# Kernel tuning notes

Measured on AMD Instinct MI355X. Metric: run time of the kernel, lower is better.

Reference implementation:

```python
import jax, jax.numpy as jnp
import numpy as np

N = 100000  # nodes
E = 1600000  # directed edges

_DIMS = [("eg1", 3, 160), ("eg2", 160, 80), ("eg3", 80, 40), ("eg4", 40, 20),
         ("el1", 20, 10), ("el2", 10, 3), ("dl1", 3, 10), ("dl2", 10, 20),
         ("dg1", 20, 40), ("dg2", 40, 80), ("dg3", 80, 160), ("dg4", 160, 3)]


def _lin_init(key, ci, co):
    s = 1.0 / np.sqrt(ci)
    kw, kb = jax.random.split(key)
    w = jax.random.uniform(kw, (ci, co), jnp.float32, -s, s)
    b = jax.random.uniform(kb, (co,), jnp.float32, -s, s)
    return w, b


def setup_inputs():
    key = jax.random.key(0)
    k0, k1, k2 = jax.random.split(key, 3)
    x = jax.random.normal(k0, (N, 3), jnp.float32)
    src = jax.random.randint(k1, (E,), 0, N)
    dst = jax.random.randint(k2, (E,), 0, N)
    edge_index = jnp.stack([src, dst])  # [2, E] int32 indices
    out = {"x": x, "edge_index": edge_index}
    for i, (name, ci, co) in enumerate(_DIMS):
        w, b = _lin_init(jax.random.fold_in(key, i + 10), ci, co)
        out[name + "_w"] = w
        out[name + "_b"] = b
    return out


def _gcn(x, w, b, src, dst, norm):
    # PyG GCNConv: linear transform, then symmetric-normalized scatter-add.
    h = x @ w
    agg = jax.ops.segment_sum(h[src] * norm[:, None], dst, num_segments=N)
    return agg + b


def reference(x, edge_index, eg1_w, eg1_b, eg2_w, eg2_b, eg3_w, eg3_b, eg4_w, eg4_b,
              el1_w, el1_b, el2_w, el2_b, dl1_w, dl1_b, dl2_w, dl2_b,
              dg1_w, dg1_b, dg2_w, dg2_b, dg3_w, dg3_b, dg4_w, dg4_b):
    loops = jnp.arange(N)
    src = jnp.concatenate([edge_index[0], loops])  # add self-loops (PyG default)
    dst = jnp.concatenate([edge_index[1], loops])
    deg = jax.ops.segment_sum(jnp.ones(src.shape[0], x.dtype), dst, num_segments=N)
    dis = jnp.where(deg > 0, jax.lax.rsqrt(deg), 0.0)
    norm = dis[src] * dis[dst]  # D^-1/2 A D^-1/2 edge weights
    relu = jax.nn.relu
    h = relu(_gcn(x, eg1_w, eg1_b, src, dst, norm))
    h = relu(_gcn(h, eg2_w, eg2_b, src, dst, norm))
    h = relu(_gcn(h, eg3_w, eg3_b, src, dst, norm))
    h = relu(_gcn(h, eg4_w, eg4_b, src, dst, norm))
    h = relu(h @ el1_w + el1_b)
    h = h @ el2_w + el2_b  # latent [N, 3]
    h = relu(h @ dl1_w + dl1_b)
    h = relu(h @ dl2_w + dl2_b)
    h = relu(_gcn(h, dg1_w, dg1_b, src, dst, norm))
    h = relu(_gcn(h, dg2_w, dg2_b, src, dst, norm))
    h = relu(_gcn(h, dg3_w, dg3_b, src, dst, norm))
    h = jnp.tanh(_gcn(h, dg4_w, dg4_b, src, dst, norm))
    return h
```

## Files before the change

### kernel.cpp

```cpp
#include <hip/hip_runtime.h>
#include <hip/hip_fp16.h>
#include <math.h>

#define BS 256
static constexpr int NN = 100000;
static constexpr int EE = 1600000;
static constexpr int BUCKET_SH = 7;
static constexpr int NBUCKET = (NN + 127) >> BUCKET_SH;
static constexpr int NB_PART = 256;
static constexpr int CHUNK = EE / NB_PART;
static constexpr int NP = NBUCKET * NB_PART;
static constexpr int SCAN_ELEMS = 1024;
static constexpr int NPB = (NP + SCAN_ELEMS - 1) / SCAN_ELEMS;

static inline int cdiv(long long a, int b) { return (int)((a + b - 1) / b); }

template <int ACT>
__device__ __forceinline__ float act_f(float v) {
    if (ACT == 1) return fmaxf(v, 0.0f);
    if (ACT == 2) return tanhf(v);
    return v;
}

__device__ __forceinline__ unsigned short h16(float v) {
    return __half_as_ushort(__float2half(v));
}
__device__ __forceinline__ unsigned pack2h(float a, float b) {
    return (unsigned)h16(a) | ((unsigned)h16(b) << 16);
}
__device__ __forceinline__ float4 cvt4h(uint2 r) {
    float2 fa = __half22float2(*(const __half2*)&r.x);
    float2 fb = __half22float2(*(const __half2*)&r.y);
    return make_float4(fa.x, fa.y, fb.x, fb.y);
}
__device__ __forceinline__ void acc8h(uint4 r, float4& a, float4& b) {
    float2 f0 = __half22float2(*(const __half2*)&r.x);
    float2 f1 = __half22float2(*(const __half2*)&r.y);
    float2 f2 = __half22float2(*(const __half2*)&r.z);
    float2 f3 = __half22float2(*(const __half2*)&r.w);
    a.x += f0.x; a.y += f0.y; a.z += f1.x; a.w += f1.y;
    b.x += f2.x; b.y += f2.y; b.z += f3.x; b.w += f3.y;
}

template <int OUTM>
__device__ __forceinline__ void store1(float* out, size_t idx, float v, float dn) {
    if (OUTM == 0) out[idx] = v;
    else if (OUTM == 1) out[idx] = v * dn;
    else if (OUTM == 2) ((unsigned short*)out)[idx] = h16(v * dn);
    else ((unsigned short*)out)[idx] = h16(v);
}

__global__ __launch_bounds__(256) void k_hist(const int* __restrict__ dst,
                                              int* __restrict__ part_cnt) {
    __shared__ int h[NBUCKET];
    int b = blockIdx.x;
    for (int j = threadIdx.x; j < NBUCKET; j += 256) h[j] = 0;
    __syncthreads();
    int e0 = b * CHUNK;
    for (int k = threadIdx.x; k < CHUNK; k += 256)
        atomicAdd(&h[dst[e0 + k] >> BUCKET_SH], 1);
    __syncthreads();
    for (int j = threadIdx.x; j < NBUCKET; j += 256)
        part_cnt[j * NB_PART + b] = h[j];
}

__global__ void k_scanA(const int* __restrict__ in, int* __restrict__ outp,
                        int* __restrict__ bsums) {
    __shared__ int lds[BS];
    int base = blockIdx.x * SCAN_ELEMS;
    int t = threadIdx.x;
    int v[4];
    int s = 0;
#pragma unroll
    for (int j = 0; j < 4; ++j) {
        int idx = base + t * 4 + j;
        v[j] = (idx < NP) ? in[idx] : 0;
        s += v[j];
    }
    lds[t] = s;
    __syncthreads();
    for (int off = 1; off < BS; off <<= 1) {
        int add = (t >= off) ? lds[t - off] : 0;
        __syncthreads();
        lds[t] += add;
        __syncthreads();
    }
    int run = lds[t] - s;
    if (t == BS - 1) bsums[blockIdx.x] = lds[BS - 1];
#pragma unroll
    for (int j = 0; j < 4; ++j) {
        int idx = base + t * 4 + j;
        if (idx < NP) outp[idx] = run;
        run += v[j];
    }
}

__global__ void k_scanB(int* __restrict__ bsums) {
    if (threadIdx.x == 0 && blockIdx.x == 0) {
        int acc = 0;
        for (int i = 0; i < NPB; ++i) {
            int t = bsums[i];
            bsums[i] = acc;
            acc += t;
        }
    }
}

__global__ void k_scanC(int* __restrict__ outp, const int* __restrict__ bsums,
                        int* __restrict__ bbase) {
    int i = blockIdx.x * BS + threadIdx.x;
    if (i < NP) {
        int v = outp[i] + bsums[i / SCAN_ELEMS];
        outp[i] = v;
        if ((i & (NB_PART - 1)) == 0) bbase[i / NB_PART] = v;
    }
    if (i == 0) bbase[NBUCKET] = EE;
}

__global__ __launch_bounds__(256) void k_part(const int* __restrict__ src,
                                              const int* __restrict__ dst,
                                              const int* __restrict__ scan_out,
                                              unsigned* __restrict__ epb) {
    __shared__ int cur[NBUCKET];
    int b = blockIdx.x;
    for (int j = threadIdx.x; j < NBUCKET; j += 256) cur[j] = scan_out[j * NB_PART + b];
    __syncthreads();
    int e0 = b * CHUNK;
    for (int k = threadIdx.x; k < CHUNK; k += 256) {
        int e = e0 + k;
        int d = dst[e];
        int s = src[e];
        int pos = atomicAdd(&cur[d >> BUCKET_SH], 1);
        epb[pos] = ((unsigned)(d & ((1 << BUCKET_SH) - 1)) << 17) | (unsigned)s;
    }
}

__global__ __launch_bounds__(256) void k_fine2(const int* __restrict__ bbase,
                                               const unsigned* __restrict__ epb,
                                               int* __restrict__ eidx,
                                               int* __restrict__ rowptr,
                                               float* __restrict__ dis) {
    __shared__ int hcnt[1 << BUCKET_SH];
    __shared__ int hoff[1 << BUCKET_SH];
    int b = blockIdx.x;
    int n0 = b << BUCKET_SH;
    int nloc = min(1 << BUCKET_SH, NN - n0);
    int t = threadIdx.x;
    if (t < (1 << BUCKET_SH)) hcnt[t] = 0;
    __syncthreads();
    int es = bbase[b], ee = bbase[b + 1];
    for (int k = es + t; k < ee; k += 256) atomicAdd(&hcnt[epb[k] >> 17], 1);
    __syncthreads();
    if (t < (1 << BUCKET_SH)) hoff[t] = hcnt[t];
    __syncthreads();
    for (int off = 1; off < (1 << BUCKET_SH); off <<= 1) {
        int add = (t >= off && t < (1 << BUCKET_SH)) ? hoff[t - off] : 0;
        __syncthreads();
        if (t < (1 << BUCKET_SH)) hoff[t] += add;
        __syncthreads();
    }
    if (t < nloc) {
        int excl = hoff[t] - hcnt[t];
        rowptr[n0 + t] = es + excl;
        dis[n0 + t] = rsqrtf((float)(hcnt[t] + 1));
    }
    __syncthreads();
    if (t < (1 << BUCKET_SH)) hoff[t] = es + hoff[t] - hcnt[t];
    __syncthreads();
    for (int k = es + t; k < ee; k += 256) {
        unsigned p = epb[k];
        int pos = atomicAdd(&hoff[p >> 17], 1);
        eidx[pos] = (int)(p & 0x1FFFFu);
    }
    if (b == NBUCKET - 1 && t == 0) rowptr[NN] = EE;
}

template <int C, int ACT, bool HASB>
__global__ void k_gatherw(const unsigned short* __restrict__ g, const int* __restrict__ rowptr,
                          const int* __restrict__ eidx, const float* __restrict__ dis,
                          const float* __restrict__ b, float* __restrict__ out) {
    static_assert(C % 8 == 0, "C%8");
    constexpr int V = C / 8;
    int t = blockIdx.x * BS + threadIdx.x;
    if (t >= NN * V) return;
    int n = t / V, v = t % V;
    const uint4* g4 = (const uint4*)g;
    float4 accA = make_float4(0.f, 0.f, 0.f, 0.f);
    float4 accB = make_float4(0.f, 0.f, 0.f, 0.f);
    acc8h(g4[(size_t)n * V + v], accA, accB);
    int rs = rowptr[n], re = rowptr[n + 1];
    int k = rs;
    for (; k + 4 <= re; k += 4) {
        int s0 = eidx[k + 0], s1 = eidx[k + 1], s2 = eidx[k + 2], s3 = eidx[k + 3];
        uint4 r0 = g4[(size_t)s0 * V + v];
        uint4 r1 = g4[(size_t)s1 * V + v];
        uint4 r2 = g4[(size_t)s2 * V + v];
        uint4 r3 = g4[(size_t)s3 * V + v];
        acc8h(r0, accA, accB);
        acc8h(r1, accA, accB);
        acc8h(r2, accA, accB);
        acc8h(r3, accA, accB);
    }
    for (; k < re; ++k) {
        acc8h(g4[(size_t)eidx[k] * V + v], accA, accB);
    }
    float dn = dis[n];
    accA.x *= dn; accA.y *= dn; accA.z *= dn; accA.w *= dn;
    accB.x *= dn; accB.y *= dn; accB.z *= dn; accB.w *= dn;
    if (HASB) {
        float4 b0 = ((const float4*)b)[v * 2 + 0];
        float4 b1 = ((const float4*)b)[v * 2 + 1];
        accA.x += b0.x; accA.y += b0.y; accA.z += b0.z; accA.w += b0.w;
        accB.x += b1.x; accB.y += b1.y; accB.z += b1.z; accB.w += b1.w;
    }
    accA.x = act_f<ACT>(accA.x); accA.y = act_f<ACT>(accA.y);
    accA.z = act_f<ACT>(accA.z); accA.w = act_f<ACT>(accA.w);
    accB.x = act_f<ACT>(accB.x); accB.y = act_f<ACT>(accB.y);
    accB.z = act_f<ACT>(accB.z); accB.w = act_f<ACT>(accB.w);
    float4* op = (float4*)out + (size_t)n * (C / 4) + v * 2;
    op[0] = accA;
    op[1] = accB;
}

template <int C, int ACT, bool HASB>
__global__ void k_gatherh(const unsigned short* __restrict__ g, const int* __restrict__ rowptr,
                          const int* __restrict__ eidx, const float* __restrict__ dis,
                          const float* __restrict__ b, float* __restrict__ out) {
    static_assert(C % 4 == 0, "C%4");
    constexpr int V = C / 4;
    int t = blockIdx.x * BS + threadIdx.x;
    if (t >= NN * V) return;
    int n = t / V, v = t % V;
    const uint2* g2 = (const uint2*)g;
    float4 acc = cvt4h(g2[(size_t)n * V + v]);
    int rs = rowptr[n], re = rowptr[n + 1];
    int k = rs;
    for (; k + 4 <= re; k += 4) {
        int s0 = eidx[k + 0], s1 = eidx[k + 1], s2 = eidx[k + 2], s3 = eidx[k + 3];
        uint2 r0 = g2[(size_t)s0 * V + v];
        uint2 r1 = g2[(size_t)s1 * V + v];
        uint2 r2 = g2[(size_t)s2 * V + v];
        uint2 r3 = g2[(size_t)s3 * V + v];
        float4 h0 = cvt4h(r0), h1 = cvt4h(r1), h2 = cvt4h(r2), h3 = cvt4h(r3);
        acc.x += (h0.x + h1.x) + (h2.x + h3.x);
        acc.y += (h0.y + h1.y) + (h2.y + h3.y);
        acc.z += (h0.z + h1.z) + (h2.z + h3.z);
        acc.w += (h0.w + h1.w) + (h2.w + h3.w);
    }
    for (; k < re; ++k) {
        float4 hv = cvt4h(g2[(size_t)eidx[k] * V + v]);
        acc.x += hv.x; acc.y += hv.y; acc.z += hv.z; acc.w += hv.w;
    }
    float dn = dis[n];
    acc.x *= dn; acc.y *= dn; acc.z *= dn; acc.w *= dn;
    if (HASB) {
        float4 bb = ((const float4*)b)[v];
        acc.x += bb.x; acc.y += bb.y; acc.z += bb.z; acc.w += bb.w;
    }
    acc.x = act_f<ACT>(acc.x);
    acc.y = act_f<ACT>(acc.y);
    acc.z = act_f<ACT>(acc.z);
    acc.w = act_f<ACT>(acc.w);
    ((float4*)out)[(size_t)n * V + v] = acc;
}

template <int ACT, bool HASB>
__global__ void k_gather3d(const float* __restrict__ g, const int* __restrict__ rowptr,
                           const int* __restrict__ eidx, const float* __restrict__ dis,
                           const float* __restrict__ b, float* __restrict__ out) {
    int n = blockIdx.x * BS + threadIdx.x;
    if (n >= NN) return;
    const float* gp = g + (size_t)n * 3;
    float a0 = gp[0], a1 = gp[1], a2 = gp[2];
    int rs = rowptr[n], re = rowptr[n + 1];
    int k = rs;
    for (; k + 4 <= re; k += 4) {
        const float* q0 = g + (size_t)eidx[k + 0] * 3;
        const float* q1 = g + (size_t)eidx[k + 1] * 3;
        const float* q2 = g + (size_t)eidx[k + 2] * 3;
        const float* q3 = g + (size_t)eidx[k + 3] * 3;
        float b00 = q0[0], b01 = q0[1], b02 = q0[2];
        float b10 = q1[0], b11 = q1[1], b12 = q1[2];
        float b20 = q2[0], b21 = q2[1], b22 = q2[2];
        float b30 = q3[0], b31 = q3[1], b32 = q3[2];
        a0 += (b00 + b10) + (b20 + b30);
        a1 += (b01 + b11) + (b21 + b31);
        a2 += (b02 + b12) + (b22 + b32);
    }
    for (; k < re; ++k) {
        const float* gq = g + (size_t)eidx[k] * 3;
        a0 += gq[0]; a1 += gq[1]; a2 += gq[2];
    }
    float dn = dis[n];
    a0 *= dn; a1 *= dn; a2 *= dn;
    if (HASB) { a0 += b[0]; a1 += b[1]; a2 += b[2]; }
    float* op = out + (size_t)n * 3;
    op[0] = act_f<ACT>(a0);
    op[1] = act_f<ACT>(a1);
    op[2] = act_f<ACT>(a2);
}

__global__ void k_scale3(const float* __restrict__ x, const float* __restrict__ dis,
                         float* __restrict__ g) {
    int i = blockIdx.x * BS + threadIdx.x;
    if (i < NN * 3) g[i] = x[i] * dis[i / 3];
}

template <int CIN, int COUT, int TC, int TN, int TM, int BK, int ACT, bool HASB, int OUTM, bool INH>
__global__ __launch_bounds__(256) void k_mm_tiled(const float* __restrict__ x,
                                                  const float* __restrict__ w,
                                                  const float* __restrict__ b,
                                                  float* __restrict__ out,
                                                  const float* __restrict__ dis) {
    constexpr int TR = 256 / TC;
    constexpr int BM = TR * TM;
    constexpr int LDA = BM + 4;
    constexpr int CHUNKS = CIN / BK;
    constexpr int BK4 = BK / 4;
    constexpr int CIN4 = CIN / 4;
    static_assert(TC * TN == COUT, "cols");
    static_assert(CIN % BK == 0 && BK % 4 == 0, "bk");
    static_assert(TM == 4 || TM == 8, "tm");
    __shared__ float As[BK * LDA];
    __shared__ float Ws[BK * COUT];
    const int tid = threadIdx.x;
    const int tc = tid % TC, tr = tid / TC;
    const int n0 = blockIdx.x * BM;

    float acc[TM][TN];
#pragma unroll
    for (int r = 0; r < TM; ++r)
#pragma unroll
        for (int j = 0; j < TN; ++j) acc[r][j] = HASB ? b[tc * TN + j] : 0.0f;

    const float4* x4 = (const float4*)x;
    const uint2* xh = (const uint2*)x;
    const float4* w4 = (const float4*)w;

    for (int ch = 0; ch < CHUNKS; ++ch) {
        const int kb4 = ch * BK4;
        if (ch) __syncthreads();
        for (int i = tid; i < BM * BK4; i += 256) {
            int r = i / BK4, k4 = i % BK4;
            int row = n0 + r;
            float4 v = make_float4(0.f, 0.f, 0.f, 0.f);
            if (row < NN) {
                if (INH) v = cvt4h(xh[(size_t)row * CIN4 + kb4 + k4]);
                else v = x4[(size_t)row * CIN4 + kb4 + k4];
            }
            int base = (4 * k4) * LDA + r;
            As[base] = v.x;
            As[base + LDA] = v.y;
            As[base + 2 * LDA] = v.z;
            As[base + 3 * LDA] = v.w;
        }
        for (int i = tid; i < BK * COUT / 4; i += 256) {
            ((float4*)Ws)[i] = w4[(size_t)kb4 * COUT + i];
        }
        __syncthreads();
#pragma unroll 4
        for (int k = 0; k < BK; ++k) {
            float a[TM];
            *(float4*)&a[0] = *(const float4*)&As[k * LDA + tr * TM];
            if (TM == 8) *(float4*)&a[4] = *(const float4*)&As[k * LDA + tr * TM + 4];
            float wr[TN];
#pragma unroll
            for (int j = 0; j < TN; ++j) wr[j] = Ws[k * COUT + tc * TN + j];
#pragma unroll
            for (int r = 0; r < TM; ++r)
#pragma unroll
                for (int j = 0; j < TN; ++j) acc[r][j] = fmaf(a[r], wr[j], acc[r][j]);
        }
    }
#pragma unroll
    for (int r = 0; r < TM; ++r) {
        int row = n0 + tr * TM + r;
        if (row < NN) {
            float dn = (OUTM == 1 || OUTM == 2) ? dis[row] : 0.0f;
            size_t base = (size_t)row * COUT + tc * TN;
#pragma unroll
            for (int j = 0; j < TN; ++j) store1<OUTM>(out, base + j, act_f<ACT>(acc[r][j]), dn);
        }
    }
}

template <int CIN, int COUT, int ACT, bool HASB, int OUTM>
__global__ void k_mm_vec4(const float* __restrict__ x, const float* __restrict__ w,
                          const float* __restrict__ b, float* __restrict__ out,
                          const float* __restrict__ dis) {
    static_assert(CIN % 4 == 0 && COUT % 4 == 0, "align");
    constexpr int TM = 8;
    constexpr int CIN4 = CIN / 4;
    constexpr int COUT4 = COUT / 4;
    constexpr int RG = NN / TM;
    int i = blockIdx.x * BS + threadIdx.x;
    if (i >= RG * COUT4) return;
    int c4 = i % COUT4;
    int n0 = (i / COUT4) * TM;
    const float4* x4 = (const float4*)x;
    const float4* w4 = (const float4*)w;
    float4 acc[TM];
    float4 bb = HASB ? ((const float4*)b)[c4] : make_float4(0.f, 0.f, 0.f, 0.f);
#pragma unroll
    for (int r = 0; r < TM; ++r) acc[r] = bb;
    for (int k4 = 0; k4 < CIN4; ++k4) {
        float4 wv[4];
#pragma unroll
        for (int j = 0; j < 4; ++j) wv[j] = w4[(size_t)(4 * k4 + j) * COUT4 + c4];
#pragma unroll
        for (int r = 0; r < TM; ++r) {
            float4 xv = x4[(size_t)(n0 + r) * CIN4 + k4];
            acc[r].x = fmaf(xv.x, wv[0].x, fmaf(xv.y, wv[1].x, fmaf(xv.z, wv[2].x, fmaf(xv.w, wv[3].x, acc[r].x))));
            acc[r].y = fmaf(xv.x, wv[0].y, fmaf(xv.y, wv[1].y, fmaf(xv.z, wv[2].y, fmaf(xv.w, wv[3].y, acc[r].y))));
            acc[r].z = fmaf(xv.x, wv[0].z, fmaf(xv.y, wv[1].z, fmaf(xv.z, wv[2].z, fmaf(xv.w, wv[3].z, acc[r].z))));
            acc[r].w = fmaf(xv.x, wv[0].w, fmaf(xv.y, wv[1].w, fmaf(xv.z, wv[2].w, fmaf(xv.w, wv[3].w, acc[r].w))));
        }
    }
#pragma unroll
    for (int r = 0; r < TM; ++r) {
        float vx = act_f<ACT>(acc[r].x), vy = act_f<ACT>(acc[r].y);
        float vz = act_f<ACT>(acc[r].z), vw = act_f<ACT>(acc[r].w);
        size_t gi = (size_t)(n0 + r) * COUT4 + c4;
        if (OUTM == 2) {
            float dn = dis[n0 + r];
            uint2 u;
            u.x = pack2h(vx * dn, vy * dn);
            u.y = pack2h(vz * dn, vw * dn);
            ((uint2*)out)[gi] = u;
        } else if (OUTM == 1) {
            float dn = dis[n0 + r];
            ((float4*)out)[gi] = make_float4(vx * dn, vy * dn, vz * dn, vw * dn);
        } else {
            ((float4*)out)[gi] = make_float4(vx, vy, vz, vw);
        }
    }
}

template <int CIN, int COUT, int ACT, int OUTM>
__global__ void k_mm_rowbcast(const float* __restrict__ x, const float* __restrict__ w,
                              const float* __restrict__ b, float* __restrict__ out) {
    static_assert(COUT % 4 == 0, "c4");
    constexpr int COUT4 = COUT / 4;
    int i = blockIdx.x * BS + threadIdx.x;
    if (i >= NN * COUT4) return;
    int n = i / COUT4, c4 = i % COUT4;
    const float4* w4 = (const float4*)w;
    float4 acc = ((const float4*)b)[c4];
    const float* xr = x + (size_t)n * CIN;
#pragma unroll
    for (int ci = 0; ci < CIN; ++ci) {
        float xv = xr[ci];
        float4 wv = w4[ci * COUT4 + c4];
        acc.x = fmaf(xv, wv.x, acc.x);
        acc.y = fmaf(xv, wv.y, acc.y);
        acc.z = fmaf(xv, wv.z, acc.z);
        acc.w = fmaf(xv, wv.w, acc.w);
    }
    acc.x = act_f<ACT>(acc.x); acc.y = act_f<ACT>(acc.y);
    acc.z = act_f<ACT>(acc.z); acc.w = act_f<ACT>(acc.w);
    if (OUTM == 3) {
        uint2 u;
        u.x = pack2h(acc.x, acc.y);
        u.y = pack2h(acc.z, acc.w);
        ((uint2*)out)[(size_t)n * COUT4 + c4] = u;
    } else {
        ((float4*)out)[(size_t)n * COUT4 + c4] = acc;
    }
}

template <int CIN, int COUT, int ACT, bool HASB, int OUTM>
__global__ void k_mm_simple(const float* __restrict__ x, const float* __restrict__ w,
                            const float* __restrict__ b, float* __restrict__ out,
                            const float* __restrict__ dis) {
    int i = blockIdx.x * BS + threadIdx.x;
    if (i >= NN * COUT) return;
    int n = i / COUT, c = i % COUT;
    const float* xr = x + (size_t)n * CIN;
    float acc = HASB ? b[c] : 0.0f;
#pragma unroll
    for (int ci = 0; ci < CIN; ++ci) acc = fmaf(xr[ci], w[ci * COUT + c], acc);
    float dn = (OUTM == 1 || OUTM == 2) ? dis[n] : 0.0f;
    store1<OUTM>(out, (size_t)i, act_f<ACT>(acc), dn);
}

template <int CIN, int COUT, int ACT, bool HASB, int OUTM, bool INH>
__global__ void k_mm_vec(const float* __restrict__ x, const float* __restrict__ w,
                         const float* __restrict__ b, float* __restrict__ out,
                         const float* __restrict__ dis) {
    static_assert(CIN % 4 == 0, "CIN%4");
    constexpr int TM = 8;
    constexpr int CIN4 = CIN / 4;
    constexpr int RG = NN / TM;
    int i = blockIdx.x * BS + threadIdx.x;
    if (i >= RG * COUT) return;
    int c = i % COUT;
    int n0 = (i / COUT) * TM;
    float acc[TM];
    float bb = HASB ? b[c] : 0.0f;
#pragma unroll
    for (int r = 0; r < TM; ++r) acc[r] = bb;
    const float4* x4 = (const float4*)x;
    const uint2* xh = (const uint2*)x;
    for (int k = 0; k < CIN4; ++k) {
        float w0 = w[(4 * k + 0) * COUT + c];
        float w1 = w[(4 * k + 1) * COUT + c];
        float w2 = w[(4 * k + 2) * COUT + c];
        float w3 = w[(4 * k + 3) * COUT + c];
#pragma unroll
        for (int r = 0; r < TM; ++r) {
            float4 xv;
            if (INH) xv = cvt4h(xh[(size_t)(n0 + r) * CIN4 + k]);
            else xv = x4[(size_t)(n0 + r) * CIN4 + k];
            acc[r] = fmaf(xv.x, w0, fmaf(xv.y, w1, fmaf(xv.z, w2, fmaf(xv.w, w3, acc[r]))));
        }
    }
#pragma unroll
    for (int r = 0; r < TM; ++r) {
        int row = n0 + r;
        float dn = (OUTM == 1 || OUTM == 2) ? dis[row] : 0.0f;
        store1<OUTM>(out, (size_t)row * COUT + c, act_f<ACT>(acc[r]), dn);
    }
}

extern "C" void kernel_launch(void* const* d_in, const int* in_sizes, int n_in,
                              void* d_out, int out_size, void* d_ws, size_t ws_size,
                              hipStream_t stream) {
    const float* x = (const float*)d_in[0];
    const int* ei = (const int*)d_in[1];
    const int* src = ei;
    const int* dst = ei + EE;
    const float* eg1_w = (const float*)d_in[2];  const float* eg1_b = (const float*)d_in[3];
    const float* eg2_w = (const float*)d_in[4];  const float* eg2_b = (const float*)d_in[5];
    const float* eg3_w = (const float*)d_in[6];  const float* eg3_b = (const float*)d_in[7];
    const float* eg4_w = (const float*)d_in[8];  const float* eg4_b = (const float*)d_in[9];
    const float* el1_w = (const float*)d_in[10]; const float* el1_b = (const float*)d_in[11];
    const float* el2_w = (const float*)d_in[12]; const float* el2_b = (const float*)d_in[13];
    const float* dl1_w = (const float*)d_in[14]; const float* dl1_b = (const float*)d_in[15];
    const float* dl2_w = (const float*)d_in[16]; const float* dl2_b = (const float*)d_in[17];
    const float* dg1_w = (const float*)d_in[18]; const float* dg1_b = (const float*)d_in[19];
    const float* dg2_w = (const float*)d_in[20]; const float* dg2_b = (const float*)d_in[21];
    const float* dg3_w = (const float*)d_in[22]; const float* dg3_b = (const float*)d_in[23];
    const float* dg4_w = (const float*)d_in[24]; const float* dg4_b = (const float*)d_in[25];
    float* out = (float*)d_out;

    char* ws = (char*)d_ws;
    size_t off = 0;
    auto alloc = [&](size_t bytes) {
        void* p = ws + off;
        off += (bytes + 15) & ~(size_t)15;
        return p;
    };
    int* part_cnt = (int*)alloc(sizeof(int) * NP);
    int* scan_out = (int*)alloc(sizeof(int) * NP);
    int* bsums    = (int*)alloc(sizeof(int) * NPB);
    int* bbase    = (int*)alloc(sizeof(int) * (NBUCKET + 1));
    int* rowptr   = (int*)alloc(sizeof(int) * (NN + 1));
    float* dis    = (float*)alloc(sizeof(float) * NN);
    int* eidx     = (int*)alloc(sizeof(int) * EE);
    unsigned* epb = (unsigned*)alloc(sizeof(unsigned) * EE);
    unsigned short* G = (unsigned short*)alloc(sizeof(unsigned short) * 80 * (size_t)NN);
    float* bufA = (float*)alloc(sizeof(float) * 160 * (size_t)NN);
    float* bufB = (float*)alloc(sizeof(float) * 160 * (size_t)NN);

    k_hist<<<NB_PART, 256, 0, stream>>>(dst, part_cnt);
    k_scanA<<<NPB, BS, 0, stream>>>(part_cnt, scan_out, bsums);
    k_scanB<<<1, 64, 0, stream>>>(bsums);
    k_scanC<<<cdiv(NP, BS), BS, 0, stream>>>(scan_out, bsums, bbase);
    k_part<<<NB_PART, 256, 0, stream>>>(src, dst, scan_out, epb);
    k_fine2<<<NBUCKET, 256, 0, stream>>>(bbase, epb, eidx, rowptr, dis);

    k_scale3<<<cdiv(3LL * NN, BS), BS, 0, stream>>>(x, dis, bufB);
    k_gather3d<0, false><<<cdiv(NN, BS), BS, 0, stream>>>(bufB, rowptr, eidx, dis, nullptr, bufA);
    k_mm_rowbcast<3, 160, 1, 3><<<cdiv(NN * 40LL, BS), BS, 0, stream>>>(bufA, eg1_w, eg1_b, bufB);

    k_mm_tiled<160, 80, 16, 5, 8, 32, 0, false, 2, true><<<cdiv(NN, 128), 256, 0, stream>>>(
        bufB, eg2_w, nullptr, (float*)G, dis);
    k_gatherw<80, 1, true><<<cdiv(NN * 10LL, BS), BS, 0, stream>>>(G, rowptr, eidx, dis, eg2_b, bufA);

    k_mm_tiled<80, 40, 8, 5, 4, 40, 0, false, 2, false><<<cdiv(NN, 128), 256, 0, stream>>>(
        bufA, eg3_w, nullptr, (float*)G, dis);
    k_gatherw<40, 1, true><<<cdiv(NN * 5LL, BS), BS, 0, stream>>>(G, rowptr, eidx, dis, eg3_b, bufB);

    k_mm_vec4<40, 20, 0, false, 2><<<cdiv((NN / 8) * 5LL, BS), BS, 0, stream>>>(
        bufB, eg4_w, nullptr, (float*)G, dis);
    k_gatherh<20, 1, true><<<cdiv(NN * 5LL, BS), BS, 0, stream>>>(G, rowptr, eidx, dis, eg4_b, bufA);

    k_mm_vec<20, 10, 1, true, 0, false><<<cdiv((NN / 8) * 10LL, BS), BS, 0, stream>>>(bufA, el1_w, el1_b, bufB, nullptr);
    k_mm_simple<10, 3, 0, true, 0><<<cdiv(3LL * NN, BS), BS, 0, stream>>>(bufB, el2_w, el2_b, bufA, nullptr);
    k_mm_simple<3, 10, 1, true, 0><<<cdiv(10LL * NN, BS), BS, 0, stream>>>(bufA, dl1_w, dl1_b, bufB, nullptr);
    k_mm_simple<10, 20, 1, true, 2><<<cdiv(20LL * NN, BS), BS, 0, stream>>>(bufB, dl2_w, dl2_b, (float*)G, dis);

    k_gatherh<20, 0, false><<<cdiv(NN * 5LL, BS), BS, 0, stream>>>(G, rowptr, eidx, dis, nullptr, bufA);
    k_mm_vec4<20, 40, 1, true, 2><<<cdiv((NN / 8) * 10LL, BS), BS, 0, stream>>>(
        bufA, dg1_w, dg1_b, (float*)G, dis);

    k_gatherw<40, 0, false><<<cdiv(NN * 5LL, BS), BS, 0, stream>>>(G, rowptr, eidx, dis, nullptr, bufB);
    k_mm_tiled<40, 80, 16, 5, 8, 40, 1, true, 2, false><<<cdiv(NN, 128), 256, 0, stream>>>(
        bufB, dg2_w, dg2_b, (float*)G, dis);

    k_gatherw<80, 0, false><<<cdiv(NN * 10LL, BS), BS, 0, stream>>>(G, rowptr, eidx, dis, nullptr, bufA);
    k_mm_tiled<80, 160, 32, 5, 8, 40, 1, true, 3, false><<<cdiv(NN, 64), 256, 0, stream>>>(
        bufA, dg3_w, dg3_b, bufB, nullptr);

    k_mm_vec<160, 3, 0, false, 1, true><<<cdiv((NN / 8) * 3LL, BS), BS, 0, stream>>>(bufB, dg4_w, nullptr, bufA, dis);
    k_gather3d<2, true><<<cdiv(NN, BS), BS, 0, stream>>>(bufA, rowptr, eidx, dis, dg4_b, out);
}
```

Measured before the change: 630.2 us.

## Store gather outputs as fp16 and fuse the latent MLP chain into one kernel

Gather kernels gain an option to write their aggregated activations as packed half precision, and the following matmul kernels read fp16 input. This roughly halves intermediate activation traffic between the gather and linear stages. The four small dense layers in the latent bottleneck are merged into one kernel that keeps weights in shared memory and intermediates in registers, which removes three launches and their round trips through global memory. The cost is more fp16 rounding of the activations, which may affect accuracy.

```diff
diff --git a/kernel.cpp b/kernel.cpp
--- a/kernel.cpp
+++ b/kernel.cpp
@@ -175,7 +175,7 @@
     if (b == NBUCKET - 1 && t == 0) rowptr[NN] = EE;
 }
 
-template <int C, int ACT, bool HASB>
+template <int C, int ACT, bool HASB, bool OUTH>
 __global__ void k_gatherw(const unsigned short* __restrict__ g, const int* __restrict__ rowptr,
                           const int* __restrict__ eidx, const float* __restrict__ dis,
                           const float* __restrict__ b, float* __restrict__ out) {
@@ -217,12 +217,21 @@
     accA.z = act_f<ACT>(accA.z); accA.w = act_f<ACT>(accA.w);
     accB.x = act_f<ACT>(accB.x); accB.y = act_f<ACT>(accB.y);
     accB.z = act_f<ACT>(accB.z); accB.w = act_f<ACT>(accB.w);
-    float4* op = (float4*)out + (size_t)n * (C / 4) + v * 2;
-    op[0] = accA;
-    op[1] = accB;
-}
-
-template <int C, int ACT, bool HASB>
+    if (OUTH) {
+        uint4 u;
+        u.x = pack2h(accA.x, accA.y);
+        u.y = pack2h(accA.z, accA.w);
+        u.z = pack2h(accB.x, accB.y);
+        u.w = pack2h(accB.z, accB.w);
+        ((uint4*)out)[(size_t)n * V + v] = u;
+    } else {
+        float4* op = (float4*)out + (size_t)n * (C / 4) + v * 2;
+        op[0] = accA;
+        op[1] = accB;
+    }
+}
+
+template <int C, int ACT, bool HASB, bool OUTH>
 __global__ void k_gatherh(const unsigned short* __restrict__ g, const int* __restrict__ rowptr,
                           const int* __restrict__ eidx, const float* __restrict__ dis,
                           const float* __restrict__ b, float* __restrict__ out) {
@@ -261,7 +270,14 @@
     acc.y = act_f<ACT>(acc.y);
     acc.z = act_f<ACT>(acc.z);
     acc.w = act_f<ACT>(acc.w);
-    ((float4*)out)[(size_t)n * V + v] = acc;
+    if (OUTH) {
+        uint2 u;
+        u.x = pack2h(acc.x, acc.y);
+        u.y = pack2h(acc.z, acc.w);
+        ((uint2*)out)[(size_t)n * V + v] = u;
+    } else {
+        ((float4*)out)[(size_t)n * V + v] = acc;
+    }
 }
 
 template <int ACT, bool HASB>
@@ -306,6 +322,78 @@
     if (i < NN * 3) g[i] = x[i] * dis[i / 3];
 }
 
+__global__ __launch_bounds__(256) void k_latent(const unsigned short* __restrict__ in20,
+                                                const float* __restrict__ el1_w, const float* __restrict__ el1_b,
+                                                const float* __restrict__ el2_w, const float* __restrict__ el2_b,
+                                                const float* __restrict__ dl1_w, const float* __restrict__ dl1_b,
+                                                const float* __restrict__ dl2_w, const float* __restrict__ dl2_b,
+                                                const float* __restrict__ dis,
+                                                unsigned short* __restrict__ G) {
+    __shared__ float w1[200], b1[10], w2[30], b2[3], w3[30], b3[10], w4[200], b4[20];
+    int t = threadIdx.x;
+    if (t < 200) w1[t] = el1_w[t];
+    if (t < 10) b1[t] = el1_b[t];
+    if (t < 30) w2[t] = el2_w[t];
+    if (t < 3) b2[t] = el2_b[t];
+    if (t < 30) w3[t] = dl1_w[t];
+    if (t < 10) b3[t] = dl1_b[t];
+    if (t < 200) w4[t] = dl2_w[t];
+    if (t < 20) b4[t] = dl2_b[t];
+    __syncthreads();
+    int n = blockIdx.x * 256 + t;
+    if (n >= NN) return;
+    float h0[20];
+    const uint2* ip = (const uint2*)in20 + (size_t)n * 5;
+#pragma unroll
+    for (int v = 0; v < 5; ++v) {
+        float4 f = cvt4h(ip[v]);
+        h0[v * 4 + 0] = f.x; h0[v * 4 + 1] = f.y;
+        h0[v * 4 + 2] = f.z; h0[v * 4 + 3] = f.w;
+    }
+    float a1[10];
+#pragma unroll
+    for (int j = 0; j < 10; ++j) {
+        float s = b1[j];
+#pragma unroll
+        for (int i = 0; i < 20; ++i) s = fmaf(h0[i], w1[i * 10 + j], s);
+        a1[j] = fmaxf(s, 0.0f);
+    }
+    float a2[3];
+#pragma unroll
+    for (int j = 0; j < 3; ++j) {
+        float s = b2[j];
+#pragma unroll
+        for (int i = 0; i < 10; ++i) s = fmaf(a1[i], w2[i * 3 + j], s);
+        a2[j] = s;
+    }
+    float a3[10];
+#pragma unroll
+    for (int j = 0; j < 10; ++j) {
+        float s = b3[j];
+#pragma unroll
+        for (int i = 0; i < 3; ++i) s = fmaf(a2[i], w3[i * 10 + j], s);
+        a3[j] = fmaxf(s, 0.0f);
+    }
+    float dn = dis[n];
+    uint2* gp = (uint2*)G + (size_t)n * 5;
+#pragma unroll
+    for (int v = 0; v < 5; ++v) {
+        float o[4];
+#pragma unroll
+        for (int q = 0; q < 4; ++q) {
+            int j = v * 4 + q;
+            float s = b4[j];
+#pragma unroll
+            for (int i = 0; i < 10; ++i) s = fmaf(a3[i], w4[i * 20 + j], s);
+            o[q] = fmaxf(s, 0.0f) * dn;
+        }
+        uint2 u;
+        u.x = pack2h(o[0], o[1]);
+        u.y = pack2h(o[2], o[3]);
+        gp[v] = u;
+    }
+}
+
 template <int CIN, int COUT, int TC, int TN, int TM, int BK, int ACT, bool HASB, int OUTM, bool INH>
 __global__ __launch_bounds__(256) void k_mm_tiled(const float* __restrict__ x,
                                                   const float* __restrict__ w,
@@ -384,7 +472,7 @@
     }
 }
 
-template <int CIN, int COUT, int ACT, bool HASB, int OUTM>
+template <int CIN, int COUT, int ACT, bool HASB, int OUTM, bool INH>
 __global__ void k_mm_vec4(const float* __restrict__ x, const float* __restrict__ w,
                           const float* __restrict__ b, float* __restrict__ out,
                           const float* __restrict__ dis) {
@@ -398,6 +486,7 @@
     int c4 = i % COUT4;
     int n0 = (i / COUT4) * TM;
     const float4* x4 = (const float4*)x;
+    const uint2* xh = (const uint2*)x;
     const float4* w4 = (const float4*)w;
     float4 acc[TM];
     float4 bb = HASB ? ((const float4*)b)[c4] : make_float4(0.f, 0.f, 0.f, 0.f);
@@ -409,7 +498,9 @@
         for (int j = 0; j < 4; ++j) wv[j] = w4[(size_t)(4 * k4 + j) * COUT4 + c4];
 #pragma unroll
         for (int r = 0; r < TM; ++r) {
-            float4 xv = x4[(size_t)(n0 + r) * CIN4 + k4];
+            float4 xv;
+            if (INH) xv = cvt4h(xh[(size_t)(n0 + r) * CIN4 + k4]);
+            else xv = x4[(size_t)(n0 + r) * CIN4 + k4];
             acc[r].x = fmaf(xv.x, wv[0].x, fmaf(xv.y, wv[1].x, fmaf(xv.z, wv[2].x, fmaf(xv.w, wv[3].x, acc[r].x))));
             acc[r].y = fmaf(xv.x, wv[0].y, fmaf(xv.y, wv[1].y, fmaf(xv.z, wv[2].y, fmaf(xv.w, wv[3].y, acc[r].y))));
             acc[r].z = fmaf(xv.x, wv[0].z, fmaf(xv.y, wv[1].z, fmaf(xv.z, wv[2].z, fmaf(xv.w, wv[3].z, acc[r].z))));
@@ -466,21 +557,6 @@
     } else {
         ((float4*)out)[(size_t)n * COUT4 + c4] = acc;
     }
-}
-
-template <int CIN, int COUT, int ACT, bool HASB, int OUTM>
-__global__ void k_mm_simple(const float* __restrict__ x, const float* __restrict__ w,
-                            const float* __restrict__ b, float* __restrict__ out,
-                            const float* __restrict__ dis) {
-    int i = blockIdx.x * BS + threadIdx.x;
-    if (i >= NN * COUT) return;
-    int n = i / COUT, c = i % COUT;
-    const float* xr = x + (size_t)n * CIN;
-    float acc = HASB ? b[c] : 0.0f;
-#pragma unroll
-    for (int ci = 0; ci < CIN; ++ci) acc = fmaf(xr[ci], w[ci * COUT + c], acc);
-    float dn = (OUTM == 1 || OUTM == 2) ? dis[n] : 0.0f;
-    store1<OUTM>(out, (size_t)i, act_f<ACT>(acc), dn);
 }
 
 template <int CIN, int COUT, int ACT, bool HASB, int OUTM, bool INH>
@@ -575,31 +651,29 @@
 
     k_mm_tiled<160, 80, 16, 5, 8, 32, 0, false, 2, true><<<cdiv(NN, 128), 256, 0, stream>>>(
         bufB, eg2_w, nullptr, (float*)G, dis);
-    k_gatherw<80, 1, true><<<cdiv(NN * 10LL, BS), BS, 0, stream>>>(G, rowptr, eidx, dis, eg2_b, bufA);
-
-    k_mm_tiled<80, 40, 8, 5, 4, 40, 0, false, 2, false><<<cdiv(NN, 128), 256, 0, stream>>>(
+    k_gatherw<80, 1, true, true><<<cdiv(NN * 10LL, BS), BS, 0, stream>>>(G, rowptr, eidx, dis, eg2_b, bufA);
+
+    k_mm_tiled<80, 40, 8, 5, 4, 40, 0, false, 2, true><<<cdiv(NN, 128), 256, 0, stream>>>(
         bufA, eg3_w, nullptr, (float*)G, dis);
-    k_gatherw<40, 1, true><<<cdiv(NN * 5LL, BS), BS, 0, stream>>>(G, rowptr, eidx, dis, eg3_b, bufB);
-
-    k_mm_vec4<40, 20, 0, false, 2><<<cdiv((NN / 8) * 5LL, BS), BS, 0, stream>>>(
+    k_gatherw<40, 1, true, true><<<cdiv(NN * 5LL, BS), BS, 0, stream>>>(G, rowptr, eidx, dis, eg3_b, bufB);
+
+    k_mm_vec4<40, 20, 0, false, 2, true><<<cdiv((NN / 8) * 5LL, BS), BS, 0, stream>>>(
         bufB, eg4_w, nullptr, (float*)G, dis);
-    k_gatherh<20, 1, true><<<cdiv(NN * 5LL, BS), BS, 0, stream>>>(G, rowptr, eidx, dis, eg4_b, bufA);
-
-    k_mm_vec<20, 10, 1, true, 0, false><<<cdiv((NN / 8) * 10LL, BS), BS, 0, stream>>>(bufA, el1_w, el1_b, bufB, nullptr);
-    k_mm_simple<10, 3, 0, true, 0><<<cdiv(3LL * NN, BS), BS, 0, stream>>>(bufB, el2_w, el2_b, bufA, nullptr);
-    k_mm_simple<3, 10, 1, true, 0><<<cdiv(10LL * NN, BS), BS, 0, stream>>>(bufA, dl1_w, dl1_b, bufB, nullptr);
-    k_mm_simple<10, 20, 1, true, 2><<<cdiv(20LL * NN, BS), BS, 0, stream>>>(bufB, dl2_w, dl2_b, (float*)G, dis);
-
-    k_gatherh<20, 0, false><<<cdiv(NN * 5LL, BS), BS, 0, stream>>>(G, rowptr, eidx, dis, nullptr, bufA);
-    k_mm_vec4<20, 40, 1, true, 2><<<cdiv((NN / 8) * 10LL, BS), BS, 0, stream>>>(
+    k_gatherh<20, 1, true, true><<<cdiv(NN * 5LL, BS), BS, 0, stream>>>(G, rowptr, eidx, dis, eg4_b, bufA);
+
+    k_latent<<<cdiv(NN, 256), 256, 0, stream>>>((const unsigned short*)bufA,
+        el1_w, el1_b, el2_w, el2_b, dl1_w, dl1_b, dl2_w, dl2_b, dis, G);
+
+    k_gatherh<20, 0, false, true><<<cdiv(NN * 5LL, BS), BS, 0, stream>>>(G, rowptr, eidx, dis, nullptr, bufA);
+    k_mm_vec4<20, 40, 1, true, 2, true><<<cdiv((NN / 8) * 10LL, BS), BS, 0, stream>>>(
         bufA, dg1_w, dg1_b, (float*)G, dis);
 
-    k_gatherw<40, 0, false><<<cdiv(NN * 5LL, BS), BS, 0, stream>>>(G, rowptr, eidx, dis, nullptr, bufB);
-    k_mm_tiled<40, 80, 16, 5, 8, 40, 1, true, 2, false><<<cdiv(NN, 128), 256, 0, stream>>>(
+    k_gatherw<40, 0, false, true><<<cdiv(NN * 5LL, BS), BS, 0, stream>>>(G, rowptr, eidx, dis, nullptr, bufB);
+    k_mm_tiled<40, 80, 16, 5, 8, 40, 1, true, 2, true><<<cdiv(NN, 128), 256, 0, stream>>>(
         bufB, dg2_w, dg2_b, (float*)G, dis);
 
-    k_gatherw<80, 0, false><<<cdiv(NN * 10LL, BS), BS, 0, stream>>>(G, rowptr, eidx, dis, nullptr, bufA);
-    k_mm_tiled<80, 160, 32, 5, 8, 40, 1, true, 3, false><<<cdiv(NN, 64), 256, 0, stream>>>(
+    k_gatherw<80, 0, false, true><<<cdiv(NN * 10LL, BS), BS, 0, stream>>>(G, rowptr, eidx, dis, nullptr, bufA);
+    k_mm_tiled<80, 160, 32, 5, 8, 40, 1, true, 3, true><<<cdiv(NN, 64), 256, 0, stream>>>(
         bufA, dg3_w, dg3_b, bufB, nullptr);
 
     k_mm_vec<160, 3, 0, false, 1, true><<<cdiv((NN / 8) * 3LL, BS), BS, 0, stream>>>(bufB, dg4_w, nullptr, bufA, dis);
```

Result: faster. 593.2 us (-5.9%).
